# Kernel optimization log

Hardware: AMD Instinct MI355X
Metric: run time of the kernel (lower is better)

The kernel has to match this reference:

```python
import jax, jax.numpy as jnp
import numpy as np

# Static config derived from init_kwargs / input shapes
N, H, W, C = 4, 224, 224, 256
F = 256            # filters
K = 3              # kernel_size
BS = 16            # block_size (input block edge)
OB = BS - K + 1    # output_block_size = 14 (valid conv of a block)
STRIDE = OB        # block_stride == output_block_size
BC = 16            # block_count = divup(224, 14) = 16
PAD = K // 2       # 'same' padding -> ZeroPadding2D(1)
TOL = 0.5


def setup_inputs() -> dict:
    key = jax.random.key(0)
    k1, k2, k3, k4 = jax.random.split(key, 4)
    inputs = jax.random.normal(k1, (N, H, W, C), jnp.float32)
    mask = jax.random.uniform(k2, (N, H, W, 1), jnp.float32)
    # learned params (kernel HWIO, bias) per glorot-ish scale
    kernel = jax.random.normal(k3, (K, K, C, F), jnp.float32) * 0.02
    bias = jax.random.normal(k4, (F,), jnp.float32) * 0.01
    return {"inputs": inputs, "mask": mask, "kernel": kernel, "bias": bias}


def reference(inputs, mask, kernel, bias):
    # 'same' path: zero-pad inputs and mask (ZeroPadding2D(pad_h=1, pad_w=1))
    pi = jnp.pad(inputs, ((0, 0), (PAD, PAD), (PAD, PAD), (0, 0)))
    pm = jnp.pad(mask, ((0, 0), (PAD, PAD), (PAD, PAD), (0, 0)))

    # block gather: input blocks of size BS at stride STRIDE (overlap K-1)
    starts = jnp.arange(BC) * STRIDE                 # [BC]
    idx = starts[:, None] + jnp.arange(BS)           # [BC, BS]
    A = idx[:, None, :, None]                        # h-index -> [BC,1,BS,1]
    B = idx[None, :, None, :]                        # w-index -> [1,BC,1,BS]
    blocks = pi[:, A, B, :]                          # [N, BC, BC, BS, BS, C]
    mblocks = pm[:, A, B, :]                         # [N, BC, BC, BS, BS, 1]

    # reduce_mask with avgpool=True: block is active iff mean(mask block) > tol
    pooled = jnp.mean(mblocks, axis=(3, 4, 5))       # [N, BC, BC]
    active = (pooled > TOL).astype(inputs.dtype)     # [N, BC, BC]

    # dense VALID conv on all blocks (equiv to conv on gathered active blocks)
    x = blocks.reshape(N * BC * BC, BS, BS, C)
    y = jax.lax.conv_general_dilated(
        x, kernel, window_strides=(1, 1), padding='VALID',
        dimension_numbers=('NHWC', 'HWIO', 'NHWC'))   # [N*BC*BC, OB, OB, F]
    y = jax.nn.relu(y + bias)

    # scatter: inactive blocks remain zero; active blocks tile output exactly
    y = y.reshape(N, BC, BC, OB, OB, F) * active[:, :, :, None, None, None]
    out = y.transpose(0, 1, 3, 2, 4, 5).reshape(N, BC * OB, BC * OB, F)
    return out  # [N, 224, 224, F]
```

## Files before the change

### kernel.cpp

```cpp
#include <hip/hip_runtime.h>
#include <hip/hip_bf16.h>

#define H 224
#define W 224
#define C 256
#define F 256
#define OB 14

typedef __attribute__((ext_vector_type(8))) short short8;
typedef __attribute__((ext_vector_type(4))) float f32x4;

__device__ __forceinline__ unsigned short f2bf(float f) {
    union { float f; unsigned u; } v; v.f = f;
    unsigned r = v.u + 0x7fffu + ((v.u >> 16) & 1u);
    return (unsigned short)(r >> 16);
}

__global__ __launch_bounds__(256) void repack_kernel(const float* __restrict__ wsrc,
                                                     unsigned short* __restrict__ wrep) {
    int g = blockIdx.x * 256 + threadIdx.x;
    int lane = g & 63;
    int nt   = (g >> 6) & 15;
    int kt   = g >> 10;
    int kk   = kt >> 3, c32 = kt & 7;
    int quad = lane >> 4, lq = lane & 15;
    int cbase = c32 * 32 + quad * 8;
    int f = nt * 16 + lq;
    alignas(16) unsigned short tmp[8];
#pragma unroll
    for (int j = 0; j < 8; ++j) {
        tmp[j] = f2bf(wsrc[((size_t)(kk * 256 + cbase + j)) * 256 + f]);
    }
    *reinterpret_cast<uint4*>(wrep + (size_t)g * 8) = *reinterpret_cast<const uint4*>(tmp);
}

__global__ void init_kernel(int* __restrict__ cnt) {
    cnt[0] = 0;
    cnt[1] = 0;
}

__global__ __launch_bounds__(256) void flags_kernel(const float* __restrict__ mask,
                                                    int* __restrict__ list,
                                                    int* __restrict__ cnt) {
    int b = blockIdx.x;
    int n = b >> 8, by = (b >> 4) & 15, bx = b & 15;
    int t = threadIdx.x;
    int r = t >> 4, s = t & 15;
    int gy = by * OB - 1 + r, gx = bx * OB - 1 + s;
    float v = 0.f;
    if ((unsigned)gy < (unsigned)H && (unsigned)gx < (unsigned)W)
        v = mask[((size_t)n * H + gy) * W + gx];
    __shared__ float red[256];
    red[t] = v;
    __syncthreads();
    if (t < 64) {
        float x = red[t] + red[t + 64] + red[t + 128] + red[t + 192];
#pragma unroll
        for (int off = 32; off; off >>= 1) x += __shfl_down(x, off);
        if (t == 0) {
            if (x > 0.5f * 256.0f) {
                int p = atomicAdd(&cnt[0], 1);
                list[p] = b;
            } else {
                int p = atomicAdd(&cnt[1], 1);
                list[1023 - p] = b;
            }
        }
    }
}

__global__ __launch_bounds__(1024, 4) void conv_kernel(const float* __restrict__ in,
                                                       const unsigned short* __restrict__ wrep,
                                                       const float* __restrict__ bias,
                                                       const int* __restrict__ list,
                                                       const int* __restrict__ cnt,
                                                       float* __restrict__ out) {
    __shared__ __align__(16) unsigned short patch[2][256 * 64];

    const int bid = blockIdx.x;
    const int n_active = cnt[0];
    const int b = list[bid];
    const int n = b >> 8, by = (b >> 4) & 15, bx = b & 15;
    const int tid = threadIdx.x;
    const int gy0 = by * OB - 1, gx0 = bx * OB - 1;
    float* outB = out + (size_t)n * H * W * F;

    if (bid >= n_active) {
#pragma unroll 4
        for (int idx = tid; idx < 196 * 64; idx += 1024) {
            int pix = idx >> 6, fv = idx & 63;
            int oy = pix / 14, ox = pix - oy * 14;
            size_t o = ((size_t)((by * OB + oy) * W + bx * OB + ox)) * F + fv * 4;
            *reinterpret_cast<float4*>(outB + o) = make_float4(0.f, 0.f, 0.f, 0.f);
        }
        return;
    }

    const int wave = tid >> 6, lane = tid & 63;
    const int quad = lane >> 4, lq = lane & 15;
    const int wm = wave >> 3;
    const int wn = wave & 7;

    const float* inB = in + (size_t)n * H * W * C;

    const float* sp[4];
    int so[4];
#pragma unroll
    for (int it = 0; it < 4; ++it) {
        int idx = tid + (it << 10);
        int pix = idx >> 4, chv = idx & 15;
        int rr = pix >> 4, ss = pix & 15;
        int gy = gy0 + rr, gx = gx0 + ss;
        bool ok = ((unsigned)gy < (unsigned)H) && ((unsigned)gx < (unsigned)W);
        sp[it] = ok ? (inB + ((size_t)(gy * W + gx)) * C + chv * 4) : nullptr;
        so[it] = (pix << 6) + (((chv >> 1) ^ (pix & 7)) << 3) + ((chv & 1) << 2);
    }

    f32x4 acc[7][2];
#pragma unroll
    for (int r = 0; r < 7; ++r) {
        acc[r][0] = (f32x4)(0.f);
        acc[r][1] = (f32x4)(0.f);
    }

    const int scol_base = (lq > 13) ? 13 : lq;
    const unsigned short* wb = wrep + ((size_t)(wn * 2) * 64 + lane) * 8;
    const int arow_base = (wm * 7 * 16) << 6;

#pragma unroll
    for (int it = 0; it < 4; ++it) {
        float4 v = make_float4(0.f, 0.f, 0.f, 0.f);
        if (sp[it]) v = *reinterpret_cast<const float4*>(sp[it]);
        uint2 bb;
        bb.x = (unsigned)f2bf(v.x) | ((unsigned)f2bf(v.y) << 16);
        bb.y = (unsigned)f2bf(v.z) | ((unsigned)f2bf(v.w) << 16);
        *reinterpret_cast<uint2*>(&patch[0][so[it]]) = bb;
    }
    __syncthreads();

    int cur = 0;
#pragma unroll 1
    for (int cc = 0; cc < 4; ++cc) {
        const bool pf = (cc < 3);
        float4 st[4];
        if (pf) {
#pragma unroll
            for (int it = 0; it < 4; ++it) {
                st[it] = make_float4(0.f, 0.f, 0.f, 0.f);
                if (sp[it]) st[it] = *reinterpret_cast<const float4*>(sp[it] + (cc + 1) * 64);
            }
        }
        const unsigned short* pc = &patch[cur][0];
#pragma unroll 1
        for (int kx = 0; kx < 3; ++kx) {
            const int scol = scol_base + kx;
            const int sw = scol & 7;
            const int acol = arow_base + (scol << 6);
#pragma unroll 1
            for (int c32l = 0; c32l < 2; ++c32l) {
                const unsigned short* ap = pc + acol + ((((c32l << 2) + quad) ^ sw) << 3);
                const unsigned short* wbk = wb + (cc * 2 + c32l) * 8192 + kx * 65536;
                short8 bf[3][2];
#pragma unroll
                for (int ky = 0; ky < 3; ++ky) {
                    bf[ky][0] = *reinterpret_cast<const short8*>(wbk + ky * 196608);
                    bf[ky][1] = *reinterpret_cast<const short8*>(wbk + ky * 196608 + 512);
                }
                __builtin_amdgcn_s_setprio(1);
#pragma unroll
                for (int rowl = 0; rowl < 9; ++rowl) {
                    short8 a = *reinterpret_cast<const short8*>(ap + (rowl << 10));
#pragma unroll
                    for (int ky = 0; ky < 3; ++ky) {
                        const int r = rowl - ky;
                        if (r >= 0 && r < 7) {
                            acc[r][0] = __builtin_amdgcn_mfma_f32_16x16x32_bf16(a, bf[ky][0], acc[r][0], 0, 0, 0);
                            acc[r][1] = __builtin_amdgcn_mfma_f32_16x16x32_bf16(a, bf[ky][1], acc[r][1], 0, 0, 0);
                        }
                    }
                }
                __builtin_amdgcn_s_setprio(0);
            }
            if (kx == 0 && pf) {
#pragma unroll
                for (int it = 0; it < 4; ++it) {
                    uint2 bb;
                    bb.x = (unsigned)f2bf(st[it].x) | ((unsigned)f2bf(st[it].y) << 16);
                    bb.y = (unsigned)f2bf(st[it].z) | ((unsigned)f2bf(st[it].w) << 16);
                    *reinterpret_cast<uint2*>(&patch[cur ^ 1][so[it]]) = bb;
                }
            }
        }
        if (pf) {
            __syncthreads();
            cur ^= 1;
        }
    }

    const float bv0 = bias[wn * 32 + lq];
    const float bv1 = bias[wn * 32 + 16 + lq];
#pragma unroll
    for (int r = 0; r < 7; ++r) {
        const int oy = wm * 7 + r;
#pragma unroll
        for (int j = 0; j < 4; ++j) {
            const int ox = quad * 4 + j;
            if (ox < 14) {
                size_t o = ((size_t)((by * OB + oy) * W + bx * OB + ox)) * F + wn * 32 + lq;
                float v0 = acc[r][0][j] + bv0;
                float v1 = acc[r][1][j] + bv1;
                outB[o]      = v0 > 0.f ? v0 : 0.f;
                outB[o + 16] = v1 > 0.f ? v1 : 0.f;
            }
        }
    }
}

extern "C" void kernel_launch(void* const* d_in, const int* in_sizes, int n_in,
                              void* d_out, int out_size, void* d_ws, size_t ws_size,
                              hipStream_t stream) {
    const float* inputs = (const float*)d_in[0];
    const float* mask   = (const float*)d_in[1];
    const float* wsrc   = (const float*)d_in[2];
    const float* bias   = (const float*)d_in[3];
    float* outp = (float*)d_out;

    unsigned short* wrep = (unsigned short*)d_ws;
    int* list = (int*)((char*)d_ws + 1179648);
    int* cnt  = (int*)((char*)d_ws + 1179648 + 4096);

    hipLaunchKernelGGL(init_kernel, dim3(1), dim3(1), 0, stream, cnt);
    hipLaunchKernelGGL(repack_kernel, dim3(288), dim3(256), 0, stream, wsrc, wrep);
    hipLaunchKernelGGL(flags_kernel, dim3(1024), dim3(256), 0, stream, mask, list, cnt);
    hipLaunchKernelGGL(conv_kernel, dim3(1024), dim3(1024), 0, stream,
                       inputs, wrep, bias, list, cnt, outp);
}
```

Before: 429.7 us.

## Halve conv workgroup to 8 waves each covering all 14 rows with prefetched weights

Shrinks the conv workgroup from 16 to 8 waves. Each wave now computes all 14 output rows for its 32 filters, so every weight fragment loaded feeds twice as many MFMAs and weight traffic per block halves. Weight fragments are double-buffered in registers (bA/bB) and loaded one step ahead of their use, and the input patch prefetch is split across the kx iterations to spread out global loads. The cost is roughly double the accumulator registers (28 f32x4 per wave), which lowers occupancy and may cause spills, and a manual lgkmcnt wait plus s_barrier replaces __syncthreads.

```diff
diff --git a/kernel.cpp b/kernel.cpp
--- a/kernel.cpp
+++ b/kernel.cpp
@@ -69,12 +69,42 @@
     }
 }
 
-__global__ __launch_bounds__(1024, 4) void conv_kernel(const float* __restrict__ in,
-                                                       const unsigned short* __restrict__ wrep,
-                                                       const float* __restrict__ bias,
-                                                       const int* __restrict__ list,
-                                                       const int* __restrict__ cnt,
-                                                       float* __restrict__ out) {
+#define LOADB(BUF, C32IDX, KXIDX)                                               \
+    do {                                                                        \
+        const unsigned short* bp_ = wb + (size_t)(C32IDX) * 8192 +              \
+                                    (size_t)(KXIDX) * 65536;                    \
+        _Pragma("unroll")                                                       \
+        for (int ky_ = 0; ky_ < 3; ++ky_) {                                     \
+            BUF[ky_][0] = *reinterpret_cast<const short8*>(bp_ + ky_ * 196608); \
+            BUF[ky_][1] = *reinterpret_cast<const short8*>(bp_ + ky_ * 196608 + 512); \
+        }                                                                       \
+    } while (0)
+
+#define HALF_MFMA(BUF, GQBASE)                                                  \
+    do {                                                                        \
+        const unsigned short* ap_ = pc + acol + ((((GQBASE) + quad) ^ sw) << 3);\
+        __builtin_amdgcn_s_setprio(1);                                          \
+        _Pragma("unroll")                                                       \
+        for (int rowl_ = 0; rowl_ < 16; ++rowl_) {                              \
+            short8 a_ = *reinterpret_cast<const short8*>(ap_ + (rowl_ << 10));  \
+            _Pragma("unroll")                                                   \
+            for (int ky_ = 0; ky_ < 3; ++ky_) {                                 \
+                const int r_ = rowl_ - ky_;                                     \
+                if (r_ >= 0 && r_ < 14) {                                       \
+                    acc[r_][0] = __builtin_amdgcn_mfma_f32_16x16x32_bf16(a_, BUF[ky_][0], acc[r_][0], 0, 0, 0); \
+                    acc[r_][1] = __builtin_amdgcn_mfma_f32_16x16x32_bf16(a_, BUF[ky_][1], acc[r_][1], 0, 0, 0); \
+                }                                                               \
+            }                                                                   \
+        }                                                                       \
+        __builtin_amdgcn_s_setprio(0);                                          \
+    } while (0)
+
+__global__ __launch_bounds__(512, 2) void conv_kernel(const float* __restrict__ in,
+                                                      const unsigned short* __restrict__ wrep,
+                                                      const float* __restrict__ bias,
+                                                      const int* __restrict__ list,
+                                                      const int* __restrict__ cnt,
+                                                      float* __restrict__ out) {
     __shared__ __align__(16) unsigned short patch[2][256 * 64];
 
     const int bid = blockIdx.x;
@@ -87,7 +117,7 @@
 
     if (bid >= n_active) {
 #pragma unroll 4
-        for (int idx = tid; idx < 196 * 64; idx += 1024) {
+        for (int idx = tid; idx < 196 * 64; idx += 512) {
             int pix = idx >> 6, fv = idx & 63;
             int oy = pix / 14, ox = pix - oy * 14;
             size_t o = ((size_t)((by * OB + oy) * W + bx * OB + ox)) * F + fv * 4;
@@ -98,101 +128,102 @@
 
     const int wave = tid >> 6, lane = tid & 63;
     const int quad = lane >> 4, lq = lane & 15;
-    const int wm = wave >> 3;
-    const int wn = wave & 7;
+    const int wn = wave;
 
     const float* inB = in + (size_t)n * H * W * C;
 
-    const float* sp[4];
-    int so[4];
-#pragma unroll
-    for (int it = 0; it < 4; ++it) {
-        int idx = tid + (it << 10);
-        int pix = idx >> 4, chv = idx & 15;
-        int rr = pix >> 4, ss = pix & 15;
-        int gy = gy0 + rr, gx = gx0 + ss;
-        bool ok = ((unsigned)gy < (unsigned)H) && ((unsigned)gx < (unsigned)W);
-        sp[it] = ok ? (inB + ((size_t)(gy * W + gx)) * C + chv * 4) : nullptr;
-        so[it] = (pix << 6) + (((chv >> 1) ^ (pix & 7)) << 3) + ((chv & 1) << 2);
-    }
-
-    f32x4 acc[7][2];
-#pragma unroll
-    for (int r = 0; r < 7; ++r) {
-        acc[r][0] = (f32x4)(0.f);
-        acc[r][1] = (f32x4)(0.f);
-    }
+    const int chv = tid & 15;
+    const int p0  = tid >> 4;
+    const int sgx = gx0 + (p0 & 15);
+    const int sr0 = p0 >> 4;
+    const bool okx = (unsigned)sgx < (unsigned)W;
+    const int so0 = (p0 << 6) + (((chv >> 1) ^ (p0 & 7)) << 3) + ((chv & 1) << 2);
+
+    f32x4 acc[14][2];
+#pragma unroll
+    for (int r = 0; r < 14; ++r) { acc[r][0] = (f32x4)(0.f); acc[r][1] = (f32x4)(0.f); }
 
     const int scol_base = (lq > 13) ? 13 : lq;
     const unsigned short* wb = wrep + ((size_t)(wn * 2) * 64 + lane) * 8;
-    const int arow_base = (wm * 7 * 16) << 6;
-
-#pragma unroll
-    for (int it = 0; it < 4; ++it) {
+
+    short8 bA[3][2], bB[3][2];
+
+#pragma unroll
+    for (int it = 0; it < 8; ++it) {
+        int gy = gy0 + sr0 + 2 * it;
         float4 v = make_float4(0.f, 0.f, 0.f, 0.f);
-        if (sp[it]) v = *reinterpret_cast<const float4*>(sp[it]);
+        if (okx && (unsigned)gy < (unsigned)H)
+            v = *reinterpret_cast<const float4*>(inB + ((size_t)gy * W + sgx) * C + chv * 4);
         uint2 bb;
         bb.x = (unsigned)f2bf(v.x) | ((unsigned)f2bf(v.y) << 16);
         bb.y = (unsigned)f2bf(v.z) | ((unsigned)f2bf(v.w) << 16);
-        *reinterpret_cast<uint2*>(&patch[0][so[it]]) = bb;
-    }
-    __syncthreads();
+        *reinterpret_cast<uint2*>(&patch[0][so0 + it * 2048]) = bb;
+    }
+    LOADB(bA, 0, 0);
+    LOADB(bB, 1, 0);
+    asm volatile("s_waitcnt lgkmcnt(0)" ::: "memory");
+    __builtin_amdgcn_s_barrier();
 
     int cur = 0;
+    float4 stA[4], stB[4];
 #pragma unroll 1
     for (int cc = 0; cc < 4; ++cc) {
-        const bool pf = (cc < 3);
-        float4 st[4];
-        if (pf) {
-#pragma unroll
-            for (int it = 0; it < 4; ++it) {
-                st[it] = make_float4(0.f, 0.f, 0.f, 0.f);
-                if (sp[it]) st[it] = *reinterpret_cast<const float4*>(sp[it] + (cc + 1) * 64);
-            }
-        }
-        const unsigned short* pc = &patch[cur][0];
+        const int pf = (cc < 3);
+        const unsigned short* pc = &patch[0][0] + cur * (256 * 64);
 #pragma unroll 1
-        for (int kx = 0; kx < 3; ++kx) {
-            const int scol = scol_base + kx;
+        for (int kx3 = 0; kx3 < 3; ++kx3) {
+            const int scol = scol_base + kx3;
             const int sw = scol & 7;
-            const int acol = arow_base + (scol << 6);
-#pragma unroll 1
-            for (int c32l = 0; c32l < 2; ++c32l) {
-                const unsigned short* ap = pc + acol + ((((c32l << 2) + quad) ^ sw) << 3);
-                const unsigned short* wbk = wb + (cc * 2 + c32l) * 8192 + kx * 65536;
-                short8 bf[3][2];
-#pragma unroll
-                for (int ky = 0; ky < 3; ++ky) {
-                    bf[ky][0] = *reinterpret_cast<const short8*>(wbk + ky * 196608);
-                    bf[ky][1] = *reinterpret_cast<const short8*>(wbk + ky * 196608 + 512);
-                }
-                __builtin_amdgcn_s_setprio(1);
-#pragma unroll
-                for (int rowl = 0; rowl < 9; ++rowl) {
-                    short8 a = *reinterpret_cast<const short8*>(ap + (rowl << 10));
-#pragma unroll
-                    for (int ky = 0; ky < 3; ++ky) {
-                        const int r = rowl - ky;
-                        if (r >= 0 && r < 7) {
-                            acc[r][0] = __builtin_amdgcn_mfma_f32_16x16x32_bf16(a, bf[ky][0], acc[r][0], 0, 0, 0);
-                            acc[r][1] = __builtin_amdgcn_mfma_f32_16x16x32_bf16(a, bf[ky][1], acc[r][1], 0, 0, 0);
-                        }
-                    }
-                }
-                __builtin_amdgcn_s_setprio(0);
-            }
-            if (kx == 0 && pf) {
+            const int acol = scol << 6;
+
+            HALF_MFMA(bA, 0);
+            if (kx3 < 2)      LOADB(bA, cc * 2, kx3 + 1);
+            else if (pf)      LOADB(bA, (cc + 1) * 2, 0);
+
+            if (kx3 == 0 && pf) {
+#pragma unroll
+                for (int it = 0; it < 4; ++it) {
+                    int gy = gy0 + sr0 + 2 * it;
+                    stA[it] = make_float4(0.f, 0.f, 0.f, 0.f);
+                    if (okx && (unsigned)gy < (unsigned)H)
+                        stA[it] = *reinterpret_cast<const float4*>(
+                            inB + ((size_t)gy * W + sgx) * C + (cc + 1) * 64 + chv * 4);
+                }
+            }
+            if (kx3 == 1 && pf) {
 #pragma unroll
                 for (int it = 0; it < 4; ++it) {
                     uint2 bb;
-                    bb.x = (unsigned)f2bf(st[it].x) | ((unsigned)f2bf(st[it].y) << 16);
-                    bb.y = (unsigned)f2bf(st[it].z) | ((unsigned)f2bf(st[it].w) << 16);
-                    *reinterpret_cast<uint2*>(&patch[cur ^ 1][so[it]]) = bb;
-                }
-            }
+                    bb.x = (unsigned)f2bf(stA[it].x) | ((unsigned)f2bf(stA[it].y) << 16);
+                    bb.y = (unsigned)f2bf(stA[it].z) | ((unsigned)f2bf(stA[it].w) << 16);
+                    *reinterpret_cast<uint2*>(&patch[cur ^ 1][so0 + it * 2048]) = bb;
+                }
+#pragma unroll
+                for (int it = 4; it < 8; ++it) {
+                    int gy = gy0 + sr0 + 2 * it;
+                    stB[it - 4] = make_float4(0.f, 0.f, 0.f, 0.f);
+                    if (okx && (unsigned)gy < (unsigned)H)
+                        stB[it - 4] = *reinterpret_cast<const float4*>(
+                            inB + ((size_t)gy * W + sgx) * C + (cc + 1) * 64 + chv * 4);
+                }
+            }
+            if (kx3 == 2 && pf) {
+#pragma unroll
+                for (int it = 4; it < 8; ++it) {
+                    uint2 bb;
+                    bb.x = (unsigned)f2bf(stB[it - 4].x) | ((unsigned)f2bf(stB[it - 4].y) << 16);
+                    bb.y = (unsigned)f2bf(stB[it - 4].z) | ((unsigned)f2bf(stB[it - 4].w) << 16);
+                    *reinterpret_cast<uint2*>(&patch[cur ^ 1][so0 + it * 2048]) = bb;
+                }
+            }
+
+            HALF_MFMA(bB, 4);
+            if (kx3 < 2)      LOADB(bB, cc * 2 + 1, kx3 + 1);
+            else if (pf)      LOADB(bB, (cc + 1) * 2 + 1, 0);
         }
         if (pf) {
-            __syncthreads();
+            asm volatile("s_waitcnt lgkmcnt(0)" ::: "memory");
+            __builtin_amdgcn_s_barrier();
             cur ^= 1;
         }
     }
@@ -200,13 +231,12 @@
     const float bv0 = bias[wn * 32 + lq];
     const float bv1 = bias[wn * 32 + 16 + lq];
 #pragma unroll
-    for (int r = 0; r < 7; ++r) {
-        const int oy = wm * 7 + r;
+    for (int r = 0; r < 14; ++r) {
 #pragma unroll
         for (int j = 0; j < 4; ++j) {
             const int ox = quad * 4 + j;
             if (ox < 14) {
-                size_t o = ((size_t)((by * OB + oy) * W + bx * OB + ox)) * F + wn * 32 + lq;
+                size_t o = ((size_t)((by * OB + r) * W + bx * OB + ox)) * F + wn * 32 + lq;
                 float v0 = acc[r][0][j] + bv0;
                 float v1 = acc[r][1][j] + bv1;
                 outB[o]      = v0 > 0.f ? v0 : 0.f;
@@ -232,6 +262,6 @@
     hipLaunchKernelGGL(init_kernel, dim3(1), dim3(1), 0, stream, cnt);
     hipLaunchKernelGGL(repack_kernel, dim3(288), dim3(256), 0, stream, wsrc, wrep);
     hipLaunchKernelGGL(flags_kernel, dim3(1024), dim3(256), 0, stream, mask, list, cnt);
-    hipLaunchKernelGGL(conv_kernel, dim3(1024), dim3(1024), 0, stream,
+    hipLaunchKernelGGL(conv_kernel, dim3(1024), dim3(512), 0, stream,
                        inputs, wrep, bias, list, cnt, outp);
 }
```

Measured after the change: 496.0 us. +15.4%, slower.

## Fuse mask reduction into conv kernel and drop flag/init launches

Applied to the files above, without the earlier changes.

Removes the init and flags kernels and computes each block's mask mean inside the conv kernel with a shared-memory reduction, so the active/inactive decision is made in place. Active and inactive blocks are no longer sorted via an atomic list. Inactive blocks now also load their first input chunk before exiting, and __syncthreads is replaced by explicit lgkmcnt waits plus s_barrier. This saves two launches and the list indirection, but gives up grouping active blocks together, so CUs may see a less even mix of heavy and light workgroups.

```diff
diff --git a/kernel.cpp b/kernel.cpp
--- a/kernel.cpp
+++ b/kernel.cpp
@@ -34,67 +34,20 @@
     *reinterpret_cast<uint4*>(wrep + (size_t)g * 8) = *reinterpret_cast<const uint4*>(tmp);
 }
 
-__global__ void init_kernel(int* __restrict__ cnt) {
-    cnt[0] = 0;
-    cnt[1] = 0;
-}
-
-__global__ __launch_bounds__(256) void flags_kernel(const float* __restrict__ mask,
-                                                    int* __restrict__ list,
-                                                    int* __restrict__ cnt) {
-    int b = blockIdx.x;
-    int n = b >> 8, by = (b >> 4) & 15, bx = b & 15;
-    int t = threadIdx.x;
-    int r = t >> 4, s = t & 15;
-    int gy = by * OB - 1 + r, gx = bx * OB - 1 + s;
-    float v = 0.f;
-    if ((unsigned)gy < (unsigned)H && (unsigned)gx < (unsigned)W)
-        v = mask[((size_t)n * H + gy) * W + gx];
-    __shared__ float red[256];
-    red[t] = v;
-    __syncthreads();
-    if (t < 64) {
-        float x = red[t] + red[t + 64] + red[t + 128] + red[t + 192];
-#pragma unroll
-        for (int off = 32; off; off >>= 1) x += __shfl_down(x, off);
-        if (t == 0) {
-            if (x > 0.5f * 256.0f) {
-                int p = atomicAdd(&cnt[0], 1);
-                list[p] = b;
-            } else {
-                int p = atomicAdd(&cnt[1], 1);
-                list[1023 - p] = b;
-            }
-        }
-    }
-}
-
 __global__ __launch_bounds__(1024, 4) void conv_kernel(const float* __restrict__ in,
                                                        const unsigned short* __restrict__ wrep,
                                                        const float* __restrict__ bias,
-                                                       const int* __restrict__ list,
-                                                       const int* __restrict__ cnt,
+                                                       const float* __restrict__ mask,
                                                        float* __restrict__ out) {
     __shared__ __align__(16) unsigned short patch[2][256 * 64];
-
-    const int bid = blockIdx.x;
-    const int n_active = cnt[0];
-    const int b = list[bid];
+    __shared__ float red[256];
+    __shared__ int s_active;
+
+    const int b = blockIdx.x;
     const int n = b >> 8, by = (b >> 4) & 15, bx = b & 15;
     const int tid = threadIdx.x;
     const int gy0 = by * OB - 1, gx0 = bx * OB - 1;
     float* outB = out + (size_t)n * H * W * F;
-
-    if (bid >= n_active) {
-#pragma unroll 4
-        for (int idx = tid; idx < 196 * 64; idx += 1024) {
-            int pix = idx >> 6, fv = idx & 63;
-            int oy = pix / 14, ox = pix - oy * 14;
-            size_t o = ((size_t)((by * OB + oy) * W + bx * OB + ox)) * F + fv * 4;
-            *reinterpret_cast<float4*>(outB + o) = make_float4(0.f, 0.f, 0.f, 0.f);
-        }
-        return;
-    }
 
     const int wave = tid >> 6, lane = tid & 63;
     const int quad = lane >> 4, lq = lane & 15;
@@ -116,16 +69,14 @@
         so[it] = (pix << 6) + (((chv >> 1) ^ (pix & 7)) << 3) + ((chv & 1) << 2);
     }
 
-    f32x4 acc[7][2];
-#pragma unroll
-    for (int r = 0; r < 7; ++r) {
-        acc[r][0] = (f32x4)(0.f);
-        acc[r][1] = (f32x4)(0.f);
-    }
-
-    const int scol_base = (lq > 13) ? 13 : lq;
-    const unsigned short* wb = wrep + ((size_t)(wn * 2) * 64 + lane) * 8;
-    const int arow_base = (wm * 7 * 16) << 6;
+    if (tid < 256) {
+        int rr = tid >> 4, ss = tid & 15;
+        int gy = gy0 + rr, gx = gx0 + ss;
+        float mv = 0.f;
+        if ((unsigned)gy < (unsigned)H && (unsigned)gx < (unsigned)W)
+            mv = mask[((size_t)n * H + gy) * W + gx];
+        red[tid] = mv;
+    }
 
 #pragma unroll
     for (int it = 0; it < 4; ++it) {
@@ -136,13 +87,42 @@
         bb.y = (unsigned)f2bf(v.z) | ((unsigned)f2bf(v.w) << 16);
         *reinterpret_cast<uint2*>(&patch[0][so[it]]) = bb;
     }
-    __syncthreads();
+    asm volatile("s_waitcnt lgkmcnt(0)" ::: "memory");
+    __builtin_amdgcn_s_barrier();
+
+    if (tid < 64) {
+        float x = red[tid] + red[tid + 64] + red[tid + 128] + red[tid + 192];
+#pragma unroll
+        for (int off = 32; off; off >>= 1) x += __shfl_down(x, off);
+        if (tid == 0) s_active = (x > 128.0f) ? 1 : 0;
+    }
+    asm volatile("s_waitcnt lgkmcnt(0)" ::: "memory");
+    __builtin_amdgcn_s_barrier();
+
+    if (!s_active) {
+#pragma unroll 4
+        for (int idx = tid; idx < 196 * 64; idx += 1024) {
+            int pix = idx >> 6, fv = idx & 63;
+            int oy = pix / 14, ox = pix - oy * 14;
+            size_t o = ((size_t)((by * OB + oy) * W + bx * OB + ox)) * F + fv * 4;
+            *reinterpret_cast<float4*>(outB + o) = make_float4(0.f, 0.f, 0.f, 0.f);
+        }
+        return;
+    }
+
+    f32x4 acc[7][2];
+#pragma unroll
+    for (int r = 0; r < 7; ++r) { acc[r][0] = (f32x4)(0.f); acc[r][1] = (f32x4)(0.f); }
+
+    const int scol_base = (lq > 13) ? 13 : lq;
+    const unsigned short* wb = wrep + ((size_t)(wn * 2) * 64 + lane) * 8;
+    const int arow_base = (wm * 7 * 16) << 6;
 
     int cur = 0;
+    float4 st[4];
 #pragma unroll 1
     for (int cc = 0; cc < 4; ++cc) {
-        const bool pf = (cc < 3);
-        float4 st[4];
+        const int pf = (cc < 3);
         if (pf) {
 #pragma unroll
             for (int it = 0; it < 4; ++it) {
@@ -150,22 +130,22 @@
                 if (sp[it]) st[it] = *reinterpret_cast<const float4*>(sp[it] + (cc + 1) * 64);
             }
         }
-        const unsigned short* pc = &patch[cur][0];
+        const unsigned short* pc = &patch[0][0] + cur * (256 * 64);
 #pragma unroll 1
-        for (int kx = 0; kx < 3; ++kx) {
-            const int scol = scol_base + kx;
+        for (int kx3 = 0; kx3 < 3; ++kx3) {
+            const int scol = scol_base + kx3;
             const int sw = scol & 7;
             const int acol = arow_base + (scol << 6);
 #pragma unroll 1
             for (int c32l = 0; c32l < 2; ++c32l) {
-                const unsigned short* ap = pc + acol + ((((c32l << 2) + quad) ^ sw) << 3);
-                const unsigned short* wbk = wb + (cc * 2 + c32l) * 8192 + kx * 65536;
+                const unsigned short* wbk = wb + (cc * 2 + c32l) * 8192 + kx3 * 65536;
                 short8 bf[3][2];
 #pragma unroll
                 for (int ky = 0; ky < 3; ++ky) {
                     bf[ky][0] = *reinterpret_cast<const short8*>(wbk + ky * 196608);
                     bf[ky][1] = *reinterpret_cast<const short8*>(wbk + ky * 196608 + 512);
                 }
+                const unsigned short* ap = pc + acol + ((((c32l << 2) + quad) ^ sw) << 3);
                 __builtin_amdgcn_s_setprio(1);
 #pragma unroll
                 for (int rowl = 0; rowl < 9; ++rowl) {
@@ -181,7 +161,7 @@
                 }
                 __builtin_amdgcn_s_setprio(0);
             }
-            if (kx == 0 && pf) {
+            if (kx3 == 0 && pf) {
 #pragma unroll
                 for (int it = 0; it < 4; ++it) {
                     uint2 bb;
@@ -192,7 +172,8 @@
             }
         }
         if (pf) {
-            __syncthreads();
+            asm volatile("s_waitcnt lgkmcnt(0)" ::: "memory");
+            __builtin_amdgcn_s_barrier();
             cur ^= 1;
         }
     }
@@ -226,12 +207,8 @@
     float* outp = (float*)d_out;
 
     unsigned short* wrep = (unsigned short*)d_ws;
-    int* list = (int*)((char*)d_ws + 1179648);
-    int* cnt  = (int*)((char*)d_ws + 1179648 + 4096);
-
-    hipLaunchKernelGGL(init_kernel, dim3(1), dim3(1), 0, stream, cnt);
+
     hipLaunchKernelGGL(repack_kernel, dim3(288), dim3(256), 0, stream, wsrc, wrep);
-    hipLaunchKernelGGL(flags_kernel, dim3(1024), dim3(256), 0, stream, mask, list, cnt);
     hipLaunchKernelGGL(conv_kernel, dim3(1024), dim3(1024), 0, stream,
-                       inputs, wrep, bias, list, cnt, outp);
-}
+                       inputs, wrep, bias, mask, outp);
+}
```

Result: slower. 465.2 us (+8.3%).
